# Kernel tuning notes

Hardware: AMD Instinct MI355X
Metric: run time of the kernel (lower is better)

Reference implementation:

```python
import jax, jax.numpy as jnp
import numpy as np

N_NODES = 100000


def _sage_conv(x, src, dst, W_l, b_l, W_r, num_nodes):
    # PyG SAGEConv (aggr='mean'): out = lin_l(mean_j x_j) + lin_r(x)
    msg = x[src]                                                   # [E, d] gather
    s = jax.ops.segment_sum(msg, dst, num_segments=num_nodes)      # [N, d]
    cnt = jax.ops.segment_sum(jnp.ones((src.shape[0], 1), x.dtype), dst,
                              num_segments=num_nodes)              # [N, 1]
    agg = s / jnp.maximum(cnt, 1)                                  # mean, 0 if no neighbors
    return agg @ W_l.T + b_l + x @ W_r.T


def setup_inputs() -> dict:
    key = jax.random.key(0)
    ks = jax.random.split(key, 8)
    d = 64
    E = 1600000
    scale = 1.0 / np.sqrt(d)
    x = jax.random.normal(ks[0], (N_NODES, d), dtype=jnp.float32)
    edge_index = jax.random.randint(ks[1], (2, E), 0, N_NODES, dtype=jnp.int64)
    W1_l = jax.random.normal(ks[2], (d, d), dtype=jnp.float32) * scale
    b1_l = jnp.zeros((d,), dtype=jnp.float32)
    W1_r = jax.random.normal(ks[3], (d, d), dtype=jnp.float32) * scale
    W2_l = jax.random.normal(ks[4], (d, d), dtype=jnp.float32) * scale
    b2_l = jnp.zeros((d,), dtype=jnp.float32)
    W2_r = jax.random.normal(ks[5], (d, d), dtype=jnp.float32) * scale
    return {"x": x, "edge_index": edge_index, "W1_l": W1_l, "b1_l": b1_l,
            "W1_r": W1_r, "W2_l": W2_l, "b2_l": b2_l, "W2_r": W2_r}


def reference(x, edge_index, W1_l, b1_l, W1_r, W2_l, b2_l, W2_r):
    src, dst = edge_index[0], edge_index[1]
    h = jax.nn.relu(_sage_conv(x, src, dst, W1_l, b1_l, W1_r, N_NODES))
    h = jax.nn.relu(_sage_conv(h, src, dst, W2_l, b2_l, W2_r, N_NODES))
    return h
```

## Files before the change

### kernel.cpp

```cpp
#include <hip/hip_runtime.h>
#include <hip/hip_fp16.h>


#define NFEAT 64
#define NPB 128
#define NBUCK 782
#define MAXPB 2560
#define TILE 4096

typedef _Float16 h8 __attribute__((ext_vector_type(8)));
typedef _Float16 h4 __attribute__((ext_vector_type(4)));
typedef float f4 __attribute__((ext_vector_type(4)));
typedef float f2 __attribute__((ext_vector_type(2)));

__device__ inline h8 cvt8f(const float* p) {
  float4 lo = *(const float4*)p;
  float4 hi = *(const float4*)(p + 4);
  h8 f;
  f[0]=(_Float16)lo.x; f[1]=(_Float16)lo.y; f[2]=(_Float16)lo.z; f[3]=(_Float16)lo.w;
  f[4]=(_Float16)hi.x; f[5]=(_Float16)hi.y; f[6]=(_Float16)hi.z; f[7]=(_Float16)hi.w;
  return f;
}

__device__ inline void acc16(float* a, uint4 r) {
  f2 t;
  t = __builtin_amdgcn_cvt_pk_f32_fp8((int)r.x, false); a[0]+=t[0];  a[1]+=t[1];
  t = __builtin_amdgcn_cvt_pk_f32_fp8((int)r.x, true);  a[2]+=t[0];  a[3]+=t[1];
  t = __builtin_amdgcn_cvt_pk_f32_fp8((int)r.y, false); a[4]+=t[0];  a[5]+=t[1];
  t = __builtin_amdgcn_cvt_pk_f32_fp8((int)r.y, true);  a[6]+=t[0];  a[7]+=t[1];
  t = __builtin_amdgcn_cvt_pk_f32_fp8((int)r.z, false); a[8]+=t[0];  a[9]+=t[1];
  t = __builtin_amdgcn_cvt_pk_f32_fp8((int)r.z, true);  a[10]+=t[0]; a[11]+=t[1];
  t = __builtin_amdgcn_cvt_pk_f32_fp8((int)r.w, false); a[12]+=t[0]; a[13]+=t[1];
  t = __builtin_amdgcn_cvt_pk_f32_fp8((int)r.w, true);  a[14]+=t[0]; a[15]+=t[1];
}

__global__ __launch_bounds__(512) void build_gemm1_k(
    const int* __restrict__ src, const int* __restrict__ dst,
    int* __restrict__ gcur, int* __restrict__ pairs, int E, int sb,
    const float* __restrict__ X, const float* __restrict__ Wl,
    const float* __restrict__ Wr, const float* __restrict__ bias,
    unsigned char* __restrict__ Zf8, __half* __restrict__ Ph, int n) {
  int tid = threadIdx.x;
  if ((int)blockIdx.x < sb) {
    __shared__ int lcnt[NBUCK];
    __shared__ int loff[NBUCK];
    __shared__ int lcur[NBUCK];
    __shared__ int lbase[NBUCK];
    __shared__ int s_packed[TILE];
    __shared__ unsigned short s_b[TILE];

    int tileStart = blockIdx.x * TILE;
    int tileCnt = E - tileStart; if (tileCnt > TILE) tileCnt = TILE;

    for (int t = tid; t < NBUCK; t += 512) lcnt[t] = 0;
    __syncthreads();

    int ep[8], eb[8];
    int base = tileStart + tid * 8;
    int ne = 0;
    if (base + 7 < E) {
      int4 a0 = *(const int4*)(src + base);
      int4 a1 = *(const int4*)(src + base + 4);
      int4 b0 = *(const int4*)(dst + base);
      int4 b1 = *(const int4*)(dst + base + 4);
      int es[8] = {a0.x,a0.y,a0.z,a0.w,a1.x,a1.y,a1.z,a1.w};
      int ed[8] = {b0.x,b0.y,b0.z,b0.w,b1.x,b1.y,b1.z,b1.w};
#pragma unroll
      for (int j = 0; j < 8; ++j) {
        eb[j] = ed[j] >> 7;
        ep[j] = es[j] | ((ed[j] & 127) << 17);
      }
      ne = 8;
    } else {
      for (int j = 0; j < 8 && base + j < E; ++j) {
        int s = src[base + j], d = dst[base + j];
        eb[j] = d >> 7;
        ep[j] = s | ((d & 127) << 17);
        ++ne;
      }
    }
    for (int j = 0; j < ne; ++j) atomicAdd(&lcnt[eb[j]], 1);
    __syncthreads();

    if (tid < 64) {
      int carry = 0;
      for (int cb = 0; cb < NBUCK; cb += 64) {
        int i = cb + tid;
        int v = (i < NBUCK) ? lcnt[i] : 0;
        int x = v;
#pragma unroll
        for (int d = 1; d < 64; d <<= 1) {
          int y = __shfl_up(x, d);
          if (tid >= d) x += y;
        }
        if (i < NBUCK) { int e = x - v + carry; loff[i] = e; lcur[i] = e; }
        carry += __shfl(x, 63);
      }
    }
    __syncthreads();

    for (int t = tid; t < NBUCK; t += 512) {
      int v = lcnt[t];
      if (v) lbase[t] = atomicAdd(&gcur[t], v);
    }
    __syncthreads();

    for (int j = 0; j < ne; ++j) {
      int b = eb[j];
      int slot = atomicAdd(&lcur[b], 1);
      s_packed[slot] = ep[j];
      s_b[slot] = (unsigned short)b;
    }
    __syncthreads();

    for (int k = tid; k < tileCnt; k += 512) {
      int b = s_b[k];
      int g = lbase[b] + (k - loff[b]);
      if (g < MAXPB) pairs[(size_t)b * MAXPB + g] = s_packed[k];
    }
  } else {
    int wave = tid >> 6, lane = tid & 63;
    int m = lane & 15, quad = lane >> 4;
    int row0 = (((int)blockIdx.x - sb) * 8 + wave) * 16;
    if (row0 >= n) return;

    h8 wf[2][4][2];
#pragma unroll
    for (int mat = 0; mat < 2; ++mat) {
      const float* W = mat ? Wr : Wl;
#pragma unroll
      for (int t = 0; t < 4; ++t)
#pragma unroll
        for (int s = 0; s < 2; ++s)
          wf[mat][t][s] = cvt8f(W + (t * 16 + m) * 64 + s * 32 + quad * 8);
    }

    int rowm = row0 + m; if (rowm > n - 1) rowm = n - 1;
    const float* xp = X + (size_t)rowm * 64 + quad * 8;
    h8 af0 = cvt8f(xp);
    h8 af1 = cvt8f(xp + 32);

    f4 accz[4], accp[4];
#pragma unroll
    for (int t = 0; t < 4; ++t) {
      f4 z; z[0]=0.f; z[1]=0.f; z[2]=0.f; z[3]=0.f;
      float4 bl = *(const float4*)(bias + t * 16 + quad * 4);
      f4 p; p[0]=bl.x; p[1]=bl.y; p[2]=bl.z; p[3]=bl.w;
      z = __builtin_amdgcn_mfma_f32_16x16x32_f16(wf[0][t][0], af0, z, 0, 0, 0);
      z = __builtin_amdgcn_mfma_f32_16x16x32_f16(wf[0][t][1], af1, z, 0, 0, 0);
      p = __builtin_amdgcn_mfma_f32_16x16x32_f16(wf[1][t][0], af0, p, 0, 0, 0);
      p = __builtin_amdgcn_mfma_f32_16x16x32_f16(wf[1][t][1], af1, p, 0, 0, 0);
      accz[t] = z;
      accp[t] = p;
    }

    if (row0 + m < n) {
      size_t node = (size_t)(row0 + m);
#pragma unroll
      for (int t = 0; t < 4; ++t) {
        h4 pv;
#pragma unroll
        for (int r = 0; r < 4; ++r) pv[r] = (_Float16)accp[t][r];
        *(h4*)(Ph + node * NFEAT + t * 16 + quad * 4) = pv;
        int v = 0;
        v = __builtin_amdgcn_cvt_pk_fp8_f32(accz[t][0], accz[t][1], v, false);
        v = __builtin_amdgcn_cvt_pk_fp8_f32(accz[t][2], accz[t][3], v, true);
        *(int*)(Zf8 + node * NFEAT + t * 16 + quad * 4) = v;
      }
    }
  }
}

__global__ __launch_bounds__(256) void regroup_k(const int* __restrict__ gcur,
                                                 const int* __restrict__ pairs,
                                                 int* __restrict__ csr,
                                                 int* __restrict__ off,
                                                 int* __restrict__ cnt,
                                                 float* __restrict__ inv, int n) {
  __shared__ int lcnt[NPB];
  __shared__ int lofs[NPB];
  __shared__ int lcur[NPB];
  __shared__ int stage[MAXPB];

  int tid = threadIdx.x;
  int b = blockIdx.x;
  int nbase = b << 7;
  int nn = n - nbase; if (nn > NPB) nn = NPB;
  if (nn <= 0) return;

  int m = gcur[b]; if (m > MAXPB) m = MAXPB;
  const int* seg = pairs + (size_t)b * MAXPB;

  if (tid < NPB) lcnt[tid] = 0;
  __syncthreads();

  for (int e = tid; e < m; e += 256)
    atomicAdd(&lcnt[(seg[e] >> 17) & 127], 1);
  __syncthreads();

  if (tid < 64) {
    int carry = 0;
#pragma unroll
    for (int cb = 0; cb < NPB; cb += 64) {
      int i = cb + tid;
      int v = lcnt[i];
      int x = v;
#pragma unroll
      for (int d = 1; d < 64; d <<= 1) {
        int y = __shfl_up(x, d);
        if (tid >= d) x += y;
      }
      int e = x - v + carry;
      lofs[i] = e; lcur[i] = e;
      carry += __shfl(x, 63);
    }
  }
  __syncthreads();

  for (int e = tid; e < m; e += 256) {
    int p = seg[e];
    int slot = atomicAdd(&lcur[(p >> 17) & 127], 1);
    stage[slot] = p & 0x1FFFF;
  }
  __syncthreads();

  for (int k = tid; k < m; k += 256) csr[(size_t)b * MAXPB + k] = stage[k];
  for (int t = tid; t < nn; t += 256) {
    int c = lcnt[t];
    cnt[nbase + t] = c;
    off[nbase + t] = b * MAXPB + lofs[t];
    inv[nbase + t] = 1.0f / (float)(c > 1 ? c : 1);
  }
}

__global__ __launch_bounds__(256) void aggemm_k(
    const int* __restrict__ off, const int* __restrict__ cnt,
    const float* __restrict__ inv, const int* __restrict__ csr,
    const unsigned char* __restrict__ Z, const __half* __restrict__ Pin,
    const float* __restrict__ Wl, const float* __restrict__ Wr,
    const float* __restrict__ bias,
    unsigned char* __restrict__ Zout, __half* __restrict__ Pout, int n) {
  __shared__ _Float16 Hs[64][72];
  int tid = threadIdx.x;
  int nbase = blockIdx.x * 64;
  int nl = tid >> 2;
  int q  = tid & 3;
  int node = nbase + nl;

  h8 h0, h1;
  if (node < n) {
    float a[16];
#pragma unroll
    for (int i = 0; i < 16; ++i) a[i] = 0.f;
    int start = off[node];
    int deg = cnt[node];
    int j = 0;
    for (; j + 4 <= deg; j += 4) {
      int n0 = csr[start + j + 0];
      int n1 = csr[start + j + 1];
      int n2 = csr[start + j + 2];
      int n3 = csr[start + j + 3];
      uint4 r0 = *(const uint4*)(Z + (size_t)n0 * NFEAT + q * 16);
      uint4 r1 = *(const uint4*)(Z + (size_t)n1 * NFEAT + q * 16);
      uint4 r2 = *(const uint4*)(Z + (size_t)n2 * NFEAT + q * 16);
      uint4 r3 = *(const uint4*)(Z + (size_t)n3 * NFEAT + q * 16);
      acc16(a, r0); acc16(a, r1); acc16(a, r2); acc16(a, r3);
    }
    for (; j < deg; ++j) {
      int nb = csr[start + j];
      uint4 r = *(const uint4*)(Z + (size_t)nb * NFEAT + q * 16);
      acc16(a, r);
    }
    float iv = inv[node];
    h8 p0 = *(const h8*)(Pin + (size_t)node * NFEAT + q * 16);
    h8 p1 = *(const h8*)(Pin + (size_t)node * NFEAT + q * 16 + 8);
#pragma unroll
    for (int i = 0; i < 8; ++i)
      h0[i] = (_Float16)fmaxf(fmaf(a[i], iv, (float)p0[i]), 0.f);
#pragma unroll
    for (int i = 0; i < 8; ++i)
      h1[i] = (_Float16)fmaxf(fmaf(a[8 + i], iv, (float)p1[i]), 0.f);
  } else {
#pragma unroll
    for (int i = 0; i < 8; ++i) { h0[i] = (_Float16)0.f; h1[i] = (_Float16)0.f; }
  }
  *(h8*)&Hs[nl][q * 16] = h0;
  *(h8*)&Hs[nl][q * 16 + 8] = h1;
  __syncthreads();

  int wave = tid >> 6, lane = tid & 63;
  int m = lane & 15, quad = lane >> 4;
  int row0 = wave * 16;

  h8 wf[2][4][2];
#pragma unroll
  for (int mat = 0; mat < 2; ++mat) {
    const float* W = mat ? Wr : Wl;
#pragma unroll
    for (int t = 0; t < 4; ++t)
#pragma unroll
      for (int s = 0; s < 2; ++s)
        wf[mat][t][s] = cvt8f(W + (t * 16 + m) * 64 + s * 32 + quad * 8);
  }

  h8 af0 = *(const h8*)&Hs[row0 + m][quad * 8];
  h8 af1 = *(const h8*)&Hs[row0 + m][32 + quad * 8];

  f4 accz[4], accp[4];
#pragma unroll
  for (int t = 0; t < 4; ++t) {
    f4 z; z[0]=0.f; z[1]=0.f; z[2]=0.f; z[3]=0.f;
    float4 bl = *(const float4*)(bias + t * 16 + quad * 4);
    f4 p; p[0]=bl.x; p[1]=bl.y; p[2]=bl.z; p[3]=bl.w;
    z = __builtin_amdgcn_mfma_f32_16x16x32_f16(wf[0][t][0], af0, z, 0, 0, 0);
    z = __builtin_amdgcn_mfma_f32_16x16x32_f16(wf[0][t][1], af1, z, 0, 0, 0);
    p = __builtin_amdgcn_mfma_f32_16x16x32_f16(wf[1][t][0], af0, p, 0, 0, 0);
    p = __builtin_amdgcn_mfma_f32_16x16x32_f16(wf[1][t][1], af1, p, 0, 0, 0);
    accz[t] = z;
    accp[t] = p;
  }

  int gnode = nbase + row0 + m;
  if (gnode < n) {
    size_t nodeix = (size_t)gnode;
#pragma unroll
    for (int t = 0; t < 4; ++t) {
      h4 pv;
#pragma unroll
      for (int r = 0; r < 4; ++r) pv[r] = (_Float16)accp[t][r];
      *(h4*)(Pout + nodeix * NFEAT + t * 16 + quad * 4) = pv;
      int v = 0;
      v = __builtin_amdgcn_cvt_pk_fp8_f32(accz[t][0], accz[t][1], v, false);
      v = __builtin_amdgcn_cvt_pk_fp8_f32(accz[t][2], accz[t][3], v, true);
      *(int*)(Zout + nodeix * NFEAT + t * 16 + quad * 4) = v;
    }
  }
}

__global__ __launch_bounds__(256) void agg2_k(const int* __restrict__ off,
                                              const int* __restrict__ cnt,
                                              const float* __restrict__ inv,
                                              const int* __restrict__ csr,
                                              const unsigned char* __restrict__ Z,
                                              const __half* __restrict__ Pin,
                                              float* __restrict__ out, int n) {
  int t = blockIdx.x * 256 + threadIdx.x;
  int node = t >> 2;
  if (node >= n) return;
  int q = t & 3;

  float a[16];
#pragma unroll
  for (int i = 0; i < 16; ++i) a[i] = 0.f;

  int start = off[node];
  int deg = cnt[node];
  int j = 0;
  for (; j + 4 <= deg; j += 4) {
    int n0 = csr[start + j + 0];
    int n1 = csr[start + j + 1];
    int n2 = csr[start + j + 2];
    int n3 = csr[start + j + 3];
    uint4 r0 = *(const uint4*)(Z + (size_t)n0 * NFEAT + q * 16);
    uint4 r1 = *(const uint4*)(Z + (size_t)n1 * NFEAT + q * 16);
    uint4 r2 = *(const uint4*)(Z + (size_t)n2 * NFEAT + q * 16);
    uint4 r3 = *(const uint4*)(Z + (size_t)n3 * NFEAT + q * 16);
    acc16(a, r0); acc16(a, r1); acc16(a, r2); acc16(a, r3);
  }
  for (; j < deg; ++j) {
    int nb = csr[start + j];
    uint4 r = *(const uint4*)(Z + (size_t)nb * NFEAT + q * 16);
    acc16(a, r);
  }

  float iv = inv[node];
  h8 p0 = *(const h8*)(Pin + (size_t)node * NFEAT + q * 16);
  h8 p1 = *(const h8*)(Pin + (size_t)node * NFEAT + q * 16 + 8);

  float4 r0, r1, r2, r3;
  r0.x = fmaxf(fmaf(a[0],  iv, (float)p0[0]), 0.f);
  r0.y = fmaxf(fmaf(a[1],  iv, (float)p0[1]), 0.f);
  r0.z = fmaxf(fmaf(a[2],  iv, (float)p0[2]), 0.f);
  r0.w = fmaxf(fmaf(a[3],  iv, (float)p0[3]), 0.f);
  r1.x = fmaxf(fmaf(a[4],  iv, (float)p0[4]), 0.f);
  r1.y = fmaxf(fmaf(a[5],  iv, (float)p0[5]), 0.f);
  r1.z = fmaxf(fmaf(a[6],  iv, (float)p0[6]), 0.f);
  r1.w = fmaxf(fmaf(a[7],  iv, (float)p0[7]), 0.f);
  r2.x = fmaxf(fmaf(a[8],  iv, (float)p1[0]), 0.f);
  r2.y = fmaxf(fmaf(a[9],  iv, (float)p1[1]), 0.f);
  r2.z = fmaxf(fmaf(a[10], iv, (float)p1[2]), 0.f);
  r2.w = fmaxf(fmaf(a[11], iv, (float)p1[3]), 0.f);
  r3.x = fmaxf(fmaf(a[12], iv, (float)p1[4]), 0.f);
  r3.y = fmaxf(fmaf(a[13], iv, (float)p1[5]), 0.f);
  r3.z = fmaxf(fmaf(a[14], iv, (float)p1[6]), 0.f);
  r3.w = fmaxf(fmaf(a[15], iv, (float)p1[7]), 0.f);

  float* op = out + (size_t)node * NFEAT + q * 16;
  *(float4*)(op + 0)  = r0;
  *(float4*)(op + 4)  = r1;
  *(float4*)(op + 8)  = r2;
  *(float4*)(op + 12) = r3;
}

extern "C" void kernel_launch(void* const* d_in, const int* in_sizes, int n_in,
                              void* d_out, int out_size, void* d_ws, size_t ws_size,
                              hipStream_t stream) {
  const float* x   = (const float*)d_in[0];
  const int*   ei  = (const int*)d_in[1];
  const float* W1l = (const float*)d_in[2];
  const float* b1  = (const float*)d_in[3];
  const float* W1r = (const float*)d_in[4];
  const float* W2l = (const float*)d_in[5];
  const float* b2  = (const float*)d_in[6];
  const float* W2r = (const float*)d_in[7];
  float* out = (float*)d_out;

  int N = in_sizes[0] / NFEAT;
  int E = in_sizes[1] / 2;
  const int* srcp = ei;
  const int* dstp = ei + E;

  char* w = (char*)d_ws;
  int*           pairs = (int*)w;           w += (size_t)NBUCK * MAXPB * 4;
  int*           csr   = (int*)w;           w += (size_t)NBUCK * MAXPB * 4;
  unsigned char* Z1    = (unsigned char*)w; w += (size_t)N * NFEAT;
  __half*        P1    = (__half*)w;        w += (size_t)N * NFEAT * 2;
  unsigned char* Z2    = (unsigned char*)w; w += (size_t)N * NFEAT;
  __half*        P2    = (__half*)w;        w += (size_t)N * NFEAT * 2;
  int*           off   = (int*)w;           w += (size_t)N * 4;
  int*           cnt   = (int*)w;           w += (size_t)N * 4;
  float*         inv   = (float*)w;         w += (size_t)N * 4;
  int*           gcur  = (int*)w;           w += NBUCK * 4;
  if ((size_t)(w - (char*)d_ws) > ws_size) return;

  hipMemsetAsync(gcur, 0, NBUCK * 4, stream);

  int sb  = (E + TILE - 1) / TILE;
  int gb1 = (N + 127) / 128;

  build_gemm1_k<<<sb + gb1, 512, 0, stream>>>(srcp, dstp, gcur, pairs, E, sb,
                                              x, W1l, W1r, b1, Z1, P1, N);
  regroup_k<<<NBUCK, 256, 0, stream>>>(gcur, pairs, csr, off, cnt, inv, N);
  aggemm_k<<<(N + 63) / 64, 256, 0, stream>>>(off, cnt, inv, csr, Z1, P1,
                                              W2l, W2r, b2, Z2, P2, N);
  agg2_k<<<(N * 4 + 255) / 256, 256, 0, stream>>>(off, cnt, inv, csr, Z2, P2,
                                                  out, N);
}
```

Before: 227.4 us.

## Fuse CSR regroup into the layer-2 aggregate+GEMM kernel using LDS neighbor lists

The bucket regroup kernel and the aggregate+GEMM kernel are merged into one 512-thread kernel per 128-node bucket. Neighbor indices, degrees and offsets are read straight from shared memory rather than from the global csr/off/cnt/inv arrays, and the inverse degree is recomputed inline. This removes one kernel launch and a global round-trip of the CSR data. The cost is more LDS per block and half as many, larger blocks, which may reduce occupancy during the latency-bound gather. The barrier before the MFMA stage is dropped because each wave only reads the Hs rows it wrote itself.

```diff
diff --git a/kernel.cpp b/kernel.cpp
--- a/kernel.cpp
+++ b/kernel.cpp
@@ -171,16 +171,19 @@
   }
 }
 
-__global__ __launch_bounds__(256) void regroup_k(const int* __restrict__ gcur,
-                                                 const int* __restrict__ pairs,
-                                                 int* __restrict__ csr,
-                                                 int* __restrict__ off,
-                                                 int* __restrict__ cnt,
-                                                 float* __restrict__ inv, int n) {
+__global__ __launch_bounds__(512) void raggemm_k(
+    const int* __restrict__ gcur, const int* __restrict__ pairs,
+    int* __restrict__ csr, int* __restrict__ off,
+    int* __restrict__ cnt, float* __restrict__ inv,
+    const unsigned char* __restrict__ Z, const __half* __restrict__ Pin,
+    const float* __restrict__ Wl, const float* __restrict__ Wr,
+    const float* __restrict__ bias,
+    unsigned char* __restrict__ Zout, __half* __restrict__ Pout, int n) {
   __shared__ int lcnt[NPB];
   __shared__ int lofs[NPB];
   __shared__ int lcur[NPB];
   __shared__ int stage[MAXPB];
+  __shared__ _Float16 Hs[NPB][72];
 
   int tid = threadIdx.x;
   int b = blockIdx.x;
@@ -194,7 +197,7 @@
   if (tid < NPB) lcnt[tid] = 0;
   __syncthreads();
 
-  for (int e = tid; e < m; e += 256)
+  for (int e = tid; e < m; e += 512)
     atomicAdd(&lcnt[(seg[e] >> 17) & 127], 1);
   __syncthreads();
 
@@ -217,32 +220,21 @@
   }
   __syncthreads();
 
-  for (int e = tid; e < m; e += 256) {
+  for (int e = tid; e < m; e += 512) {
     int p = seg[e];
     int slot = atomicAdd(&lcur[(p >> 17) & 127], 1);
     stage[slot] = p & 0x1FFFF;
   }
   __syncthreads();
 
-  for (int k = tid; k < m; k += 256) csr[(size_t)b * MAXPB + k] = stage[k];
-  for (int t = tid; t < nn; t += 256) {
+  for (int k = tid; k < m; k += 512) csr[(size_t)b * MAXPB + k] = stage[k];
+  for (int t = tid; t < nn; t += 512) {
     int c = lcnt[t];
     cnt[nbase + t] = c;
     off[nbase + t] = b * MAXPB + lofs[t];
     inv[nbase + t] = 1.0f / (float)(c > 1 ? c : 1);
   }
-}
-
-__global__ __launch_bounds__(256) void aggemm_k(
-    const int* __restrict__ off, const int* __restrict__ cnt,
-    const float* __restrict__ inv, const int* __restrict__ csr,
-    const unsigned char* __restrict__ Z, const __half* __restrict__ Pin,
-    const float* __restrict__ Wl, const float* __restrict__ Wr,
-    const float* __restrict__ bias,
-    unsigned char* __restrict__ Zout, __half* __restrict__ Pout, int n) {
-  __shared__ _Float16 Hs[64][72];
-  int tid = threadIdx.x;
-  int nbase = blockIdx.x * 64;
+
   int nl = tid >> 2;
   int q  = tid & 3;
   int node = nbase + nl;
@@ -252,14 +244,14 @@
     float a[16];
 #pragma unroll
     for (int i = 0; i < 16; ++i) a[i] = 0.f;
-    int start = off[node];
-    int deg = cnt[node];
+    int deg = lcnt[nl];
+    int start = lofs[nl];
     int j = 0;
     for (; j + 4 <= deg; j += 4) {
-      int n0 = csr[start + j + 0];
-      int n1 = csr[start + j + 1];
-      int n2 = csr[start + j + 2];
-      int n3 = csr[start + j + 3];
+      int n0 = stage[start + j + 0];
+      int n1 = stage[start + j + 1];
+      int n2 = stage[start + j + 2];
+      int n3 = stage[start + j + 3];
       uint4 r0 = *(const uint4*)(Z + (size_t)n0 * NFEAT + q * 16);
       uint4 r1 = *(const uint4*)(Z + (size_t)n1 * NFEAT + q * 16);
       uint4 r2 = *(const uint4*)(Z + (size_t)n2 * NFEAT + q * 16);
@@ -267,11 +259,11 @@
       acc16(a, r0); acc16(a, r1); acc16(a, r2); acc16(a, r3);
     }
     for (; j < deg; ++j) {
-      int nb = csr[start + j];
+      int nb = stage[start + j];
       uint4 r = *(const uint4*)(Z + (size_t)nb * NFEAT + q * 16);
       acc16(a, r);
     }
-    float iv = inv[node];
+    float iv = 1.0f / (float)(deg > 1 ? deg : 1);
     h8 p0 = *(const h8*)(Pin + (size_t)node * NFEAT + q * 16);
     h8 p1 = *(const h8*)(Pin + (size_t)node * NFEAT + q * 16 + 8);
 #pragma unroll
@@ -286,10 +278,9 @@
   }
   *(h8*)&Hs[nl][q * 16] = h0;
   *(h8*)&Hs[nl][q * 16 + 8] = h1;
-  __syncthreads();
 
   int wave = tid >> 6, lane = tid & 63;
-  int m = lane & 15, quad = lane >> 4;
+  int mm = lane & 15, quad = lane >> 4;
   int row0 = wave * 16;
 
   h8 wf[2][4][2];
@@ -300,11 +291,11 @@
     for (int t = 0; t < 4; ++t)
 #pragma unroll
       for (int s = 0; s < 2; ++s)
-        wf[mat][t][s] = cvt8f(W + (t * 16 + m) * 64 + s * 32 + quad * 8);
-  }
-
-  h8 af0 = *(const h8*)&Hs[row0 + m][quad * 8];
-  h8 af1 = *(const h8*)&Hs[row0 + m][32 + quad * 8];
+        wf[mat][t][s] = cvt8f(W + (t * 16 + mm) * 64 + s * 32 + quad * 8);
+  }
+
+  h8 af0 = *(const h8*)&Hs[row0 + mm][quad * 8];
+  h8 af1 = *(const h8*)&Hs[row0 + mm][32 + quad * 8];
 
   f4 accz[4], accp[4];
 #pragma unroll
@@ -320,7 +311,7 @@
     accp[t] = p;
   }
 
-  int gnode = nbase + row0 + m;
+  int gnode = nbase + row0 + mm;
   if (gnode < n) {
     size_t nodeix = (size_t)gnode;
 #pragma unroll
@@ -440,9 +431,8 @@
 
   build_gemm1_k<<<sb + gb1, 512, 0, stream>>>(srcp, dstp, gcur, pairs, E, sb,
                                               x, W1l, W1r, b1, Z1, P1, N);
-  regroup_k<<<NBUCK, 256, 0, stream>>>(gcur, pairs, csr, off, cnt, inv, N);
-  aggemm_k<<<(N + 63) / 64, 256, 0, stream>>>(off, cnt, inv, csr, Z1, P1,
-                                              W2l, W2r, b2, Z2, P2, N);
+  raggemm_k<<<NBUCK, 512, 0, stream>>>(gcur, pairs, csr, off, cnt, inv,
+                                       Z1, P1, W2l, W2r, b2, Z2, P2, N);
   agg2_k<<<(N * 4 + 255) / 256, 256, 0, stream>>>(off, cnt, inv, csr, Z2, P2,
                                                   out, N);
 }
```

Measured after the change: 227.0 us. No clear change (-0.2%).
